# Kernel tuning notes

Hardware: AMD Instinct MI355X
Metric: run time of the kernel (lower is better)

## Reference

```python
import jax, jax.numpy as jnp
import numpy as np

K = 512  # number of largest entries to KEEP per row (module's k)


def _topk_keep(x, k):
    """Zero all but the k largest entries along the last axis.

    Matches torch: topk(-x, dim-k) finds the (dim-k) smallest values of x
    and scatters 0 into them, keeping the k largest. We implement the
    equivalent keep-mask via top_k indices of x itself (ties resolved by
    index order, same as torch.topk).
    """
    shp = x.shape
    d = shp[-1]
    x2 = x.reshape(-1, d)                      # [N, d]
    _, idx = jax.lax.top_k(x2, k)              # [N, k] indices of largest
    rows = jnp.arange(x2.shape[0])[:, None]    # [N, 1]
    mask = jnp.zeros_like(x2).at[rows, idx].set(1.0)
    return (x2 * mask).reshape(shp)


def setup_inputs() -> dict:
    key = jax.random.key(0)
    x = jax.random.normal(key, (4, 4096, 4096), dtype=jnp.float32)
    return {"x": x}


def reference(x):
    return _topk_keep(x, K)
```

## Files before the change

kernel.cpp:

```cpp
#include <hip/hip_runtime.h>

#define D     4096
#define KKEEP 512
#define TPB   256
#define NSEG  4
#define NB    2048
#define BPT   (NB / TPB)
#define HA(d) ((d) + ((d) >> 3))
#define HWORDS (NB + NB / 8)

__device__ __forceinline__ unsigned key_of(float f) {
    unsigned u = __float_as_uint(f);
    return (u & 0x80000000u) ? ~u : (u | 0x80000000u);
}
__device__ __forceinline__ float val_of(unsigned k) {
    unsigned u = (k & 0x80000000u) ? (k ^ 0x80000000u) : ~k;
    return __uint_as_float(u);
}

__global__ __launch_bounds__(TPB, 8)
void topk_keep_kernel(const float* __restrict__ x, float* __restrict__ out) {
    const int tid = threadIdx.x;
    const unsigned lane = tid & 63u, wid = (unsigned)tid >> 6;
    const float4* px = (const float4*)(x + (long)blockIdx.x * D);
    float4*       po = (float4*)(out + (long)blockIdx.x * D);

    unsigned k[NSEG * 4];
    {
        float4 f0 = px[tid], f1 = px[tid + TPB], f2 = px[tid + 2 * TPB], f3 = px[tid + 3 * TPB];
        k[ 0]=key_of(f0.x); k[ 1]=key_of(f0.y); k[ 2]=key_of(f0.z); k[ 3]=key_of(f0.w);
        k[ 4]=key_of(f1.x); k[ 5]=key_of(f1.y); k[ 6]=key_of(f1.z); k[ 7]=key_of(f1.w);
        k[ 8]=key_of(f2.x); k[ 9]=key_of(f2.y); k[10]=key_of(f2.z); k[11]=key_of(f2.w);
        k[12]=key_of(f3.x); k[13]=key_of(f3.y); k[14]=key_of(f3.z); k[15]=key_of(f3.w);
    }

    __shared__ unsigned hist[HWORDS];
    __shared__ unsigned s_wtot[4];
    __shared__ unsigned s_sel[2];
    __shared__ unsigned s_w01[4];
    __shared__ unsigned s_w23[4];

    #pragma unroll
    for (int i = 0; i < 9; ++i) hist[tid + i * TPB] = 0;
    __syncthreads();

    unsigned prefix = 0;
    unsigned rem = KKEEP;

    #pragma unroll
    for (int r = 0; r < 3; ++r) {
        const int shift = (r == 0) ? 21 : (r == 1) ? 10 : 0;
        const unsigned mask = (r == 2) ? 1023u : 2047u;

        if (r == 0) {
            #pragma unroll
            for (int j = 0; j < 16; ++j)
                atomicAdd(&hist[HA(k[j] >> 21)], 1u);
        } else {
            const int hs = (r == 1) ? 21 : 10;
            #pragma unroll
            for (int j = 0; j < 16; ++j)
                if ((k[j] >> hs) == (prefix >> hs))
                    atomicAdd(&hist[HA((k[j] >> shift) & mask)], 1u);
        }
        __syncthreads();

        unsigned c[BPT];
        unsigned ct = 0;
        {
            const int hb = tid * 9;
            #pragma unroll
            for (int i = 0; i < BPT; ++i) { c[i] = hist[hb + i]; ct += c[i]; }
            if (r < 2) {
                #pragma unroll
                for (int i = 0; i < BPT; ++i) hist[hb + i] = 0;
            }
        }
        unsigned s = ct;
        #pragma unroll
        for (int off = 1; off < 64; off <<= 1) {
            unsigned t = __shfl_down(s, off, 64);
            if (lane + (unsigned)off < 64u) s += t;
        }
        if (lane == 0) s_wtot[wid] = s;
        __syncthreads();
        unsigned above = s - ct;
        #pragma unroll
        for (unsigned w = 0; w < 4; ++w)
            if (w > wid) above += s_wtot[w];
        unsigned run = above;
        #pragma unroll
        for (int i = BPT - 1; i >= 0; --i) {
            unsigned incl = run + c[i];
            if (incl >= rem && run < rem) {
                s_sel[0] = (unsigned)(tid * BPT + i);
                s_sel[1] = rem - run;
            }
            run = incl;
        }
        __syncthreads();
        prefix |= s_sel[0] << shift;
        rem = s_sel[1];
    }

    const unsigned tkey = prefix;

    unsigned e[NSEG];
    #pragma unroll
    for (int j = 0; j < NSEG; ++j) {
        unsigned c0 = (k[4*j+0] == tkey), c1 = (k[4*j+1] == tkey);
        unsigned c2 = (k[4*j+2] == tkey), c3 = (k[4*j+3] == tkey);
        e[j] = c0 + c1 + c2 + c3;
    }
    unsigned p01 = e[0] | (e[1] << 16);
    unsigned p23 = e[2] | (e[3] << 16);
    unsigned i01 = p01, i23 = p23;
    #pragma unroll
    for (int off = 1; off < 64; off <<= 1) {
        unsigned t0 = __shfl_up(i01, off, 64);
        unsigned t1 = __shfl_up(i23, off, 64);
        if (lane >= (unsigned)off) { i01 += t0; i23 += t1; }
    }
    if (lane == 63) { s_w01[wid] = i01; s_w23[wid] = i23; }
    __syncthreads();
    unsigned x01 = i01 - p01, x23 = i23 - p23;
    #pragma unroll
    for (unsigned w = 0; w < 4; ++w)
        if (w < wid) { x01 += s_w01[w]; x23 += s_w23[w]; }
    const unsigned tot01 = s_w01[0] + s_w01[1] + s_w01[2] + s_w01[3];
    const unsigned tot23 = s_w23[0] + s_w23[1] + s_w23[2] + s_w23[3];
    const unsigned total0 = tot01 & 0xffffu, total1 = tot01 >> 16;
    const unsigned total2 = tot23 & 0xffffu;
    unsigned rank[NSEG];
    rank[0] = (x01 & 0xffffu);
    rank[1] = total0 + (x01 >> 16);
    rank[2] = total0 + total1 + (x23 & 0xffffu);
    rank[3] = total0 + total1 + total2 + (x23 >> 16);

    #pragma unroll
    for (int j = 0; j < NSEG; ++j) {
        float4 o;
        unsigned eqr = rank[j];
        float* ofp = (float*)&o;
        #pragma unroll
        for (int c = 0; c < 4; ++c) {
            unsigned kk = k[4*j + c];
            bool keep;
            if (kk > tkey)       keep = true;
            else if (kk == tkey) { keep = (eqr < rem); ++eqr; }
            else                 keep = false;
            ofp[c] = keep ? val_of(kk) : 0.0f;
        }
        po[tid + j * TPB] = o;
    }
}

extern "C" void kernel_launch(void* const* d_in, const int* in_sizes, int n_in,
                              void* d_out, int out_size, void* d_ws, size_t ws_size,
                              hipStream_t stream) {
    const float* x = (const float*)d_in[0];
    float* out = (float*)d_out;
    const int rows = in_sizes[0] / D;
    topk_keep_kernel<<<dim3(rows), dim3(TPB), 0, stream>>>(x, out);
}
```

Baseline: 431.5 us.

## Process multiple rows per block with next-row prefetch and tie fast path

```diff
diff --git a/kernel.cpp b/kernel.cpp
--- a/kernel.cpp
+++ b/kernel.cpp
@@ -8,150 +8,183 @@
 #define BPT   (NB / TPB)
 #define HA(d) ((d) + ((d) >> 3))
 #define HWORDS (NB + NB / 8)
+#define RPB   8
 
 __device__ __forceinline__ unsigned key_of(float f) {
     unsigned u = __float_as_uint(f);
-    return (u & 0x80000000u) ? ~u : (u | 0x80000000u);
+    return u ^ ((unsigned)((int)u >> 31) | 0x80000000u);
 }
 __device__ __forceinline__ float val_of(unsigned k) {
     unsigned u = (k & 0x80000000u) ? (k ^ 0x80000000u) : ~k;
     return __uint_as_float(u);
 }
 
-__global__ __launch_bounds__(TPB, 8)
+__device__ __forceinline__ void bar_lds() {
+    asm volatile("s_waitcnt lgkmcnt(0)" ::: "memory");
+    __builtin_amdgcn_s_barrier();
+    asm volatile("" ::: "memory");
+}
+
+__global__ __launch_bounds__(TPB, 7)
 void topk_keep_kernel(const float* __restrict__ x, float* __restrict__ out) {
     const int tid = threadIdx.x;
     const unsigned lane = tid & 63u, wid = (unsigned)tid >> 6;
-    const float4* px = (const float4*)(x + (long)blockIdx.x * D);
-    float4*       po = (float4*)(out + (long)blockIdx.x * D);
-
-    unsigned k[NSEG * 4];
-    {
-        float4 f0 = px[tid], f1 = px[tid + TPB], f2 = px[tid + 2 * TPB], f3 = px[tid + 3 * TPB];
-        k[ 0]=key_of(f0.x); k[ 1]=key_of(f0.y); k[ 2]=key_of(f0.z); k[ 3]=key_of(f0.w);
-        k[ 4]=key_of(f1.x); k[ 5]=key_of(f1.y); k[ 6]=key_of(f1.z); k[ 7]=key_of(f1.w);
-        k[ 8]=key_of(f2.x); k[ 9]=key_of(f2.y); k[10]=key_of(f2.z); k[11]=key_of(f2.w);
-        k[12]=key_of(f3.x); k[13]=key_of(f3.y); k[14]=key_of(f3.z); k[15]=key_of(f3.w);
-    }
+    const long row0 = (long)blockIdx.x * RPB;
+    const float4* px = (const float4*)(x + row0 * D);
+    float4*       po = (float4*)(out + row0 * D);
 
     __shared__ unsigned hist[HWORDS];
     __shared__ unsigned s_wtot[4];
-    __shared__ unsigned s_sel[2];
+    __shared__ unsigned s_sel[3];
     __shared__ unsigned s_w01[4];
     __shared__ unsigned s_w23[4];
 
     #pragma unroll
     for (int i = 0; i < 9; ++i) hist[tid + i * TPB] = 0;
-    __syncthreads();
 
-    unsigned prefix = 0;
-    unsigned rem = KKEEP;
+    float4 f0 = px[tid], f1 = px[tid + TPB], f2 = px[tid + 2 * TPB], f3 = px[tid + 3 * TPB];
+    bar_lds();
 
-    #pragma unroll
-    for (int r = 0; r < 3; ++r) {
-        const int shift = (r == 0) ? 21 : (r == 1) ? 10 : 0;
-        const unsigned mask = (r == 2) ? 1023u : 2047u;
+    #pragma unroll 1
+    for (int row = 0; row < RPB; ++row) {
+        unsigned k[NSEG * 4];
+        k[ 0]=key_of(f0.x); k[ 1]=key_of(f0.y); k[ 2]=key_of(f0.z); k[ 3]=key_of(f0.w);
+        k[ 4]=key_of(f1.x); k[ 5]=key_of(f1.y); k[ 6]=key_of(f1.z); k[ 7]=key_of(f1.w);
+        k[ 8]=key_of(f2.x); k[ 9]=key_of(f2.y); k[10]=key_of(f2.z); k[11]=key_of(f2.w);
+        k[12]=key_of(f3.x); k[13]=key_of(f3.y); k[14]=key_of(f3.z); k[15]=key_of(f3.w);
 
-        if (r == 0) {
-            #pragma unroll
-            for (int j = 0; j < 16; ++j)
-                atomicAdd(&hist[HA(k[j] >> 21)], 1u);
-        } else {
-            const int hs = (r == 1) ? 21 : 10;
-            #pragma unroll
-            for (int j = 0; j < 16; ++j)
-                if ((k[j] >> hs) == (prefix >> hs))
-                    atomicAdd(&hist[HA((k[j] >> shift) & mask)], 1u);
+        if (row + 1 < RPB) {
+            const float4* pn = px + (long)(row + 1) * (D / 4);
+            f0 = pn[tid]; f1 = pn[tid + TPB]; f2 = pn[tid + 2 * TPB]; f3 = pn[tid + 3 * TPB];
         }
-        __syncthreads();
 
-        unsigned c[BPT];
-        unsigned ct = 0;
-        {
-            const int hb = tid * 9;
-            #pragma unroll
-            for (int i = 0; i < BPT; ++i) { c[i] = hist[hb + i]; ct += c[i]; }
-            if (r < 2) {
+        unsigned prefix = 0;
+        unsigned rem = KKEEP;
+        unsigned eqn = 0;
+
+        #pragma unroll
+        for (int r = 0; r < 3; ++r) {
+            const int shift = (r == 0) ? 21 : (r == 1) ? 10 : 0;
+            const unsigned mask = (r == 2) ? 1023u : 2047u;
+
+            if (r == 0) {
+                #pragma unroll
+                for (int j = 0; j < 16; ++j)
+                    atomicAdd(&hist[HA(k[j] >> 21)], 1u);
+            } else {
+                const int hs = (r == 1) ? 21 : 10;
+                #pragma unroll
+                for (int j = 0; j < 16; ++j)
+                    if ((k[j] >> hs) == (prefix >> hs))
+                        atomicAdd(&hist[HA((k[j] >> shift) & mask)], 1u);
+            }
+            bar_lds();
+
+            unsigned c[BPT];
+            unsigned ct = 0;
+            {
+                const int hb = tid * 9;
+                #pragma unroll
+                for (int i = 0; i < BPT; ++i) { c[i] = hist[hb + i]; ct += c[i]; }
                 #pragma unroll
                 for (int i = 0; i < BPT; ++i) hist[hb + i] = 0;
             }
+            unsigned s = ct;
+            #pragma unroll
+            for (int off = 1; off < 64; off <<= 1) {
+                unsigned t = __shfl_down(s, off, 64);
+                if (lane + (unsigned)off < 64u) s += t;
+            }
+            if (lane == 0) s_wtot[wid] = s;
+            bar_lds();
+            unsigned above = s - ct;
+            #pragma unroll
+            for (unsigned w = 0; w < 4; ++w)
+                if (w > wid) above += s_wtot[w];
+            unsigned run = above;
+            #pragma unroll
+            for (int i = BPT - 1; i >= 0; --i) {
+                unsigned incl = run + c[i];
+                if (incl >= rem && run < rem) {
+                    s_sel[0] = (unsigned)(tid * BPT + i);
+                    s_sel[1] = rem - run;
+                    s_sel[2] = c[i];
+                }
+                run = incl;
+            }
+            bar_lds();
+            prefix |= s_sel[0] << shift;
+            rem = s_sel[1];
+            eqn = s_sel[2];
         }
-        unsigned s = ct;
+
+        const unsigned tkey = prefix;
+        float4* por = po + (long)row * (D / 4);
+
+        if (rem == eqn) {
+            #pragma unroll
+            for (int j = 0; j < NSEG; ++j) {
+                float4 o;
+                float* ofp = (float*)&o;
+                #pragma unroll
+                for (int c = 0; c < 4; ++c) {
+                    const unsigned kk = k[4 * j + c];
+                    ofp[c] = (kk >= tkey) ? val_of(kk) : 0.0f;
+                }
+                por[tid + j * TPB] = o;
+            }
+            continue;
+        }
+
+        unsigned e[NSEG];
+        #pragma unroll
+        for (int j = 0; j < NSEG; ++j) {
+            unsigned c0 = (k[4*j+0] == tkey), c1 = (k[4*j+1] == tkey);
+            unsigned c2 = (k[4*j+2] == tkey), c3 = (k[4*j+3] == tkey);
+            e[j] = c0 + c1 + c2 + c3;
+        }
+        unsigned p01 = e[0] | (e[1] << 16);
+        unsigned p23 = e[2] | (e[3] << 16);
+        unsigned i01 = p01, i23 = p23;
         #pragma unroll
         for (int off = 1; off < 64; off <<= 1) {
-            unsigned t = __shfl_down(s, off, 64);
-            if (lane + (unsigned)off < 64u) s += t;
+            unsigned t0 = __shfl_up(i01, off, 64);
+            unsigned t1 = __shfl_up(i23, off, 64);
+            if (lane >= (unsigned)off) { i01 += t0; i23 += t1; }
         }
-        if (lane == 0) s_wtot[wid] = s;
-        __syncthreads();
-        unsigned above = s - ct;
+        if (lane == 63) { s_w01[wid] = i01; s_w23[wid] = i23; }
+        bar_lds();
+        unsigned x01 = i01 - p01, x23 = i23 - p23;
         #pragma unroll
         for (unsigned w = 0; w < 4; ++w)
-            if (w > wid) above += s_wtot[w];
-        unsigned run = above;
+            if (w < wid) { x01 += s_w01[w]; x23 += s_w23[w]; }
+        const unsigned tot01 = s_w01[0] + s_w01[1] + s_w01[2] + s_w01[3];
+        const unsigned tot23 = s_w23[0] + s_w23[1] + s_w23[2] + s_w23[3];
+        const unsigned total0 = tot01 & 0xffffu, total1 = tot01 >> 16;
+        const unsigned total2 = tot23 & 0xffffu;
+        unsigned rank[NSEG];
+        rank[0] = (x01 & 0xffffu);
+        rank[1] = total0 + (x01 >> 16);
+        rank[2] = total0 + total1 + (x23 & 0xffffu);
+        rank[3] = total0 + total1 + total2 + (x23 >> 16);
+        bar_lds();
+
         #pragma unroll
-        for (int i = BPT - 1; i >= 0; --i) {
-            unsigned incl = run + c[i];
-            if (incl >= rem && run < rem) {
-                s_sel[0] = (unsigned)(tid * BPT + i);
-                s_sel[1] = rem - run;
+        for (int j = 0; j < NSEG; ++j) {
+            float4 o;
+            unsigned eqr = rank[j];
+            float* ofp = (float*)&o;
+            #pragma unroll
+            for (int c = 0; c < 4; ++c) {
+                const unsigned kk = k[4 * j + c];
+                bool keep;
+                if (kk > tkey)       keep = true;
+                else if (kk == tkey) { keep = (eqr < rem); ++eqr; }
+                else                 keep = false;
+                ofp[c] = keep ? val_of(kk) : 0.0f;
             }
-            run = incl;
+            por[tid + j * TPB] = o;
         }
-        __syncthreads();
-        prefix |= s_sel[0] << shift;
-        rem = s_sel[1];
-    }
-
-    const unsigned tkey = prefix;
-
-    unsigned e[NSEG];
-    #pragma unroll
-    for (int j = 0; j < NSEG; ++j) {
-        unsigned c0 = (k[4*j+0] == tkey), c1 = (k[4*j+1] == tkey);
-        unsigned c2 = (k[4*j+2] == tkey), c3 = (k[4*j+3] == tkey);
-        e[j] = c0 + c1 + c2 + c3;
-    }
-    unsigned p01 = e[0] | (e[1] << 16);
-    unsigned p23 = e[2] | (e[3] << 16);
-    unsigned i01 = p01, i23 = p23;
-    #pragma unroll
-    for (int off = 1; off < 64; off <<= 1) {
-        unsigned t0 = __shfl_up(i01, off, 64);
-        unsigned t1 = __shfl_up(i23, off, 64);
-        if (lane >= (unsigned)off) { i01 += t0; i23 += t1; }
-    }
-    if (lane == 63) { s_w01[wid] = i01; s_w23[wid] = i23; }
-    __syncthreads();
-    unsigned x01 = i01 - p01, x23 = i23 - p23;
-    #pragma unroll
-    for (unsigned w = 0; w < 4; ++w)
-        if (w < wid) { x01 += s_w01[w]; x23 += s_w23[w]; }
-    const unsigned tot01 = s_w01[0] + s_w01[1] + s_w01[2] + s_w01[3];
-    const unsigned tot23 = s_w23[0] + s_w23[1] + s_w23[2] + s_w23[3];
-    const unsigned total0 = tot01 & 0xffffu, total1 = tot01 >> 16;
-    const unsigned total2 = tot23 & 0xffffu;
-    unsigned rank[NSEG];
-    rank[0] = (x01 & 0xffffu);
-    rank[1] = total0 + (x01 >> 16);
-    rank[2] = total0 + total1 + (x23 & 0xffffu);
-    rank[3] = total0 + total1 + total2 + (x23 >> 16);
-
-    #pragma unroll
-    for (int j = 0; j < NSEG; ++j) {
-        float4 o;
-        unsigned eqr = rank[j];
-        float* ofp = (float*)&o;
-        #pragma unroll
-        for (int c = 0; c < 4; ++c) {
-            unsigned kk = k[4*j + c];
-            bool keep;
-            if (kk > tkey)       keep = true;
-            else if (kk == tkey) { keep = (eqr < rem); ++eqr; }
-            else                 keep = false;
-            ofp[c] = keep ? val_of(kk) : 0.0f;
-        }
-        po[tid + j * TPB] = o;
     }
 }
 
@@ -161,5 +194,6 @@
     const float* x = (const float*)d_in[0];
     float* out = (float*)d_out;
     const int rows = in_sizes[0] / D;
-    topk_keep_kernel<<<dim3(rows), dim3(TPB), 0, stream>>>(x, out);
+    const int blocks = rows / RPB;
+    topk_keep_kernel<<<dim3(blocks), dim3(TPB), 0, stream>>>(x, out);
 }
```

Measured after the change: 518.3 us. +20.1%, slower.
